# Kernel tuning notes

Measured on AMD Instinct MI355X. Metric: run time of the kernel, lower is better.

The kernel has to match this reference:

```python
import jax, jax.numpy as jnp
import numpy as np

B = 64        # number of bags
D = 512       # feature dim
T = 131072    # total instances across all bags (ragged, avg ~2048/bag)


def setup_inputs() -> dict:
    key = jax.random.key(0)
    k_s, _ = jax.random.split(key)
    samples = jax.random.normal(k_s, (T, D), dtype=jnp.float32)
    # Ragged bag sizes that sum exactly to T (deterministic).
    rng = np.random.default_rng(0)
    w = rng.random(B)
    counts = np.floor(w / w.sum() * T).astype(np.int64)
    counts = np.maximum(counts, 1)
    counts[-1] += T - counts.sum()
    bags_num_samples = jnp.asarray(counts, dtype=jnp.int64)
    return {"samples": samples, "bags_num_samples": bags_num_samples}


def reference(samples, bags_num_samples):
    # Fused segmented mean-pool replacing the per-bag Python loop:
    # bag i owns rows [cum[i-1], cum[i]) of `samples`.
    n_bags = bags_num_samples.shape[0]
    total = samples.shape[0]
    seg_ids = jnp.repeat(jnp.arange(n_bags), bags_num_samples,
                         total_repeat_length=total)  # [T]
    sums = jax.ops.segment_sum(samples, seg_ids, num_segments=n_bags)  # [B, D]
    return sums / bags_num_samples[:, None].astype(samples.dtype)
```

## Files before the change

kernel.cpp:

```cpp
#include <hip/hip_runtime.h>

#define NBAGS 64
#define D 512
#define D4 128
#define RPC 128
#define TTOT 131072
#define MAXCHUNKS (TTOT / RPC + NBAGS)

__global__ void agg_partial_kernel(const float* __restrict__ samples,
                                   const int* __restrict__ counts,
                                   float* __restrict__ partials) {
    const int g = blockIdx.x;

    int bag = -1, mychunk = 0;
    long long rowbase = 0, cnt = 0;
    {
        long long cb = 0, rb = 0;
#pragma unroll
        for (int i = 0; i < NBAGS; ++i) {
            long long c  = (long long)counts[i];
            int       nc = (int)((c + RPC - 1) / RPC);
            if (bag < 0 && g >= cb && g < cb + nc) {
                bag = i; mychunk = (int)(g - cb); rowbase = rb; cnt = c;
            }
            cb += nc; rb += c;
        }
    }
    if (bag < 0) return;

    const long long r0 = rowbase + (long long)mychunk * RPC;
    const long long r1 = min(rowbase + cnt, r0 + (long long)RPC);

    const int t    = threadIdx.x;
    const int col  = t & (D4 - 1);
    const int half = t >> 7;

    const float4* __restrict__ src = (const float4*)samples;

    float4 a0 = make_float4(0.f, 0.f, 0.f, 0.f);
    float4 a1 = make_float4(0.f, 0.f, 0.f, 0.f);
    long long r = r0 + half;
    for (; r + 6 < r1; r += 8) {
        float4 v0 = src[(r    ) * D4 + col];
        float4 v1 = src[(r + 2) * D4 + col];
        float4 v2 = src[(r + 4) * D4 + col];
        float4 v3 = src[(r + 6) * D4 + col];
        a0.x += v0.x; a0.y += v0.y; a0.z += v0.z; a0.w += v0.w;
        a1.x += v1.x; a1.y += v1.y; a1.z += v1.z; a1.w += v1.w;
        a0.x += v2.x; a0.y += v2.y; a0.z += v2.z; a0.w += v2.w;
        a1.x += v3.x; a1.y += v3.y; a1.z += v3.z; a1.w += v3.w;
    }
    for (; r < r1; r += 2) {
        float4 v = src[r * D4 + col];
        a0.x += v.x; a0.y += v.y; a0.z += v.z; a0.w += v.w;
    }
    a0.x += a1.x; a0.y += a1.y; a0.z += a1.z; a0.w += a1.w;

    __shared__ float4 lds[D4];
    if (half == 1) lds[col] = a0;
    __syncthreads();
    if (half == 0) {
        float4 o = lds[col];
        a0.x += o.x; a0.y += o.y; a0.z += o.z; a0.w += o.w;
        ((float4*)partials)[(long long)g * D4 + col] = a0;
    }
}

__global__ void agg_reduce_kernel(const float* __restrict__ partials,
                                  const int* __restrict__ counts,
                                  float* __restrict__ out) {
    const int bag = blockIdx.x;
    const int col = threadIdx.x;

    long long cb = 0; int nc = 0; long long cnt = 0;
#pragma unroll
    for (int i = 0; i < NBAGS; ++i) {
        long long c  = (long long)counts[i];
        int       n  = (int)((c + RPC - 1) / RPC);
        if (i == bag) { nc = n; cnt = c; break; }
        cb += n;
    }

    const float4* __restrict__ p = (const float4*)partials;
    float4 acc = make_float4(0.f, 0.f, 0.f, 0.f);
    for (int c = 0; c < nc; ++c) {
        float4 v = p[(cb + c) * D4 + col];
        acc.x += v.x; acc.y += v.y; acc.z += v.z; acc.w += v.w;
    }
    const float inv = 1.0f / (float)cnt;
    acc.x *= inv; acc.y *= inv; acc.z *= inv; acc.w *= inv;
    ((float4*)out)[bag * D4 + col] = acc;
}

extern "C" void kernel_launch(void* const* d_in, const int* in_sizes, int n_in,
                              void* d_out, int out_size, void* d_ws, size_t ws_size,
                              hipStream_t stream) {
    const float* samples  = (const float*)d_in[0];
    const int*   counts   = (const int*)d_in[1];
    float*       out      = (float*)d_out;
    float*       partials = (float*)d_ws;

    agg_partial_kernel<<<MAXCHUNKS, 256, 0, stream>>>(samples, counts, partials);
    agg_reduce_kernel<<<NBAGS, D4, 0, stream>>>(partials, counts, out);
}
```

Before: 58.80 us.

## Balance chunk partitioning across bags and compute chunk map with wave scans

Replaces fixed 128-row chunks (about 1088 blocks, many partially filled) with a proportional split into roughly 1024 chunks of near-equal row counts. Each block's bag and row range now come from a 64-lane wave scan over the counts instead of a serial 64-iteration loop per thread. The aim is to cut per-block setup latency and even out load, at the cost of longer chunks per block and a shared-memory sync. It also switches to 32-bit indexing and reads the total row count from in_sizes.

Measured after the change: 56.21 us. -4.4%, faster.

```diff
diff --git a/kernel.cpp b/kernel.cpp
--- a/kernel.cpp
+++ b/kernel.cpp
@@ -3,35 +3,50 @@
 #define NBAGS 64
 #define D 512
 #define D4 128
-#define RPC 128
-#define TTOT 131072
-#define MAXCHUNKS (TTOT / RPC + NBAGS)
+#define TARGET_CHUNKS 1024
+#define GRID1 1088
 
-__global__ void agg_partial_kernel(const float* __restrict__ samples,
-                                   const int* __restrict__ counts,
-                                   float* __restrict__ partials) {
+
+__device__ __forceinline__ int lane_incl_scan(int v, int lane) {
+#pragma unroll
+    for (int off = 1; off < 64; off <<= 1) {
+        int o = __shfl_up(v, off, 64);
+        if (lane >= off) v += o;
+    }
+    return v;
+}
+
+__global__ __launch_bounds__(256) void
+agg_partial_kernel(const float* __restrict__ samples,
+                   const int* __restrict__ counts,
+                   float* __restrict__ partials, int tt) {
+    __shared__ int s_bag, s_r0, s_r1;
+    const int t = threadIdx.x;
     const int g = blockIdx.x;
 
-    int bag = -1, mychunk = 0;
-    long long rowbase = 0, cnt = 0;
-    {
-        long long cb = 0, rb = 0;
+    if (t == 0) s_bag = -1;
+    if (t < 64) {
+        const int c = counts[t];
+        int n = (c * TARGET_CHUNKS) / tt;
+        if (n < 1) n = 1;
+        int S = n;
 #pragma unroll
-        for (int i = 0; i < NBAGS; ++i) {
-            long long c  = (long long)counts[i];
-            int       nc = (int)((c + RPC - 1) / RPC);
-            if (bag < 0 && g >= cb && g < cb + nc) {
-                bag = i; mychunk = (int)(g - cb); rowbase = rb; cnt = c;
-            }
-            cb += nc; rb += c;
+        for (int m = 1; m < 64; m <<= 1) S += __shfl_xor(S, m, 64);
+        int L = TARGET_CHUNKS - S; if (L < 0) L = 0;
+        n += (t < L) ? 1 : 0;
+        const int cb = lane_incl_scan(n, t) - n;
+        const int rb = lane_incl_scan(c, t) - c;
+        if (g >= cb && g < cb + n) {
+            const int j = g - cb;
+            s_bag = t;
+            s_r0 = rb + (c * j) / n;
+            s_r1 = rb + (c * (j + 1)) / n;
         }
     }
-    if (bag < 0) return;
+    __syncthreads();
+    if (s_bag < 0) return;
+    const int r0 = s_r0, r1 = s_r1;
 
-    const long long r0 = rowbase + (long long)mychunk * RPC;
-    const long long r1 = min(rowbase + cnt, r0 + (long long)RPC);
-
-    const int t    = threadIdx.x;
     const int col  = t & (D4 - 1);
     const int half = t >> 7;
 
@@ -39,7 +54,7 @@
 
     float4 a0 = make_float4(0.f, 0.f, 0.f, 0.f);
     float4 a1 = make_float4(0.f, 0.f, 0.f, 0.f);
-    long long r = r0 + half;
+    int r = r0 + half;
     for (; r + 6 < r1; r += 8) {
         float4 v0 = src[(r    ) * D4 + col];
         float4 v1 = src[(r + 2) * D4 + col];
@@ -62,34 +77,42 @@
     if (half == 0) {
         float4 o = lds[col];
         a0.x += o.x; a0.y += o.y; a0.z += o.z; a0.w += o.w;
-        ((float4*)partials)[(long long)g * D4 + col] = a0;
+        ((float4*)partials)[g * D4 + col] = a0;
     }
 }
 
-__global__ void agg_reduce_kernel(const float* __restrict__ partials,
-                                  const int* __restrict__ counts,
-                                  float* __restrict__ out) {
+__global__ __launch_bounds__(D4) void
+agg_reduce_kernel(const float* __restrict__ partials,
+                  const int* __restrict__ counts,
+                  float* __restrict__ out, int tt) {
+    __shared__ int s_cb, s_n;
+    const int t   = threadIdx.x;
     const int bag = blockIdx.x;
-    const int col = threadIdx.x;
 
-    long long cb = 0; int nc = 0; long long cnt = 0;
+    if (t < 64) {
+        const int c = counts[t];
+        int n = (c * TARGET_CHUNKS) / tt;
+        if (n < 1) n = 1;
+        int S = n;
 #pragma unroll
-    for (int i = 0; i < NBAGS; ++i) {
-        long long c  = (long long)counts[i];
-        int       n  = (int)((c + RPC - 1) / RPC);
-        if (i == bag) { nc = n; cnt = c; break; }
-        cb += n;
+        for (int m = 1; m < 64; m <<= 1) S += __shfl_xor(S, m, 64);
+        int L = TARGET_CHUNKS - S; if (L < 0) L = 0;
+        n += (t < L) ? 1 : 0;
+        const int cb = lane_incl_scan(n, t) - n;
+        if (t == bag) { s_cb = cb; s_n = n; }
     }
+    __syncthreads();
+    const int cb = s_cb, n = s_n;
 
     const float4* __restrict__ p = (const float4*)partials;
     float4 acc = make_float4(0.f, 0.f, 0.f, 0.f);
-    for (int c = 0; c < nc; ++c) {
-        float4 v = p[(cb + c) * D4 + col];
+    for (int k = 0; k < n; ++k) {
+        float4 v = p[(cb + k) * D4 + t];
         acc.x += v.x; acc.y += v.y; acc.z += v.z; acc.w += v.w;
     }
-    const float inv = 1.0f / (float)cnt;
+    const float inv = 1.0f / (float)counts[bag];
     acc.x *= inv; acc.y *= inv; acc.z *= inv; acc.w *= inv;
-    ((float4*)out)[bag * D4 + col] = acc;
+    ((float4*)out)[bag * D4 + t] = acc;
 }
 
 extern "C" void kernel_launch(void* const* d_in, const int* in_sizes, int n_in,
@@ -99,7 +122,8 @@
     const int*   counts   = (const int*)d_in[1];
     float*       out      = (float*)d_out;
     float*       partials = (float*)d_ws;
+    const int    tt       = in_sizes[0] / D;
 
-    agg_partial_kernel<<<MAXCHUNKS, 256, 0, stream>>>(samples, counts, partials);
-    agg_reduce_kernel<<<NBAGS, D4, 0, stream>>>(partials, counts, out);
+    agg_partial_kernel<<<GRID1, 256, 0, stream>>>(samples, counts, partials, tt);
+    agg_reduce_kernel<<<NBAGS, D4, 0, stream>>>(partials, counts, out, tt);
 }
```
